# Kernel tuning notes

Hardware: AMD Instinct MI355X
Metric: run time of the kernel (lower is better)

The kernel has to match this reference:

```python
import jax, jax.numpy as jnp
import numpy as np

B, C, T, N, KS = 32, 64, 12, 1024, 3
OUT = 64


def _gconv_layer(x, Lk, theta, b):
    # x: [B, i, T, N], Lk: [ks, N, N], theta: [i, c, ks], b: [1, c, 1, 1]
    x_c = jnp.einsum('knm,bitm->bitkn', Lk, x)        # graph diffusion
    x_gc = jnp.einsum('iok,bitkn->botn', theta, x_c) + b  # channel mix + bias
    return jax.nn.relu(x_gc + x)                      # residual + relu


def setup_inputs() -> dict:
    key = jax.random.key(0)
    ks = jax.random.split(key, 8)
    return {
        'x': jax.random.normal(ks[0], (B, C, T, N), dtype=jnp.float32),
        'Lk': jax.random.normal(ks[1], (KS, N, N), dtype=jnp.float32) * 0.05,
        'theta1': jax.random.normal(ks[2], (C, C, KS), dtype=jnp.float32) * 0.1,
        'b1': jax.random.normal(ks[3], (1, C, 1, 1), dtype=jnp.float32) * 0.1,
        'theta2': jax.random.normal(ks[4], (C, C, KS), dtype=jnp.float32) * 0.1,
        'b2': jax.random.normal(ks[5], (1, C, 1, 1), dtype=jnp.float32) * 0.1,
        'fc_w': jax.random.normal(ks[6], (OUT, C), dtype=jnp.float32) * 0.1,
        'fc_b': jax.random.normal(ks[7], (OUT,), dtype=jnp.float32) * 0.1,
    }


def reference(x, Lk, theta1, b1, theta2, b2, fc_w, fc_b):
    x1 = _gconv_layer(x, Lk, theta1, b1)
    x2 = _gconv_layer(x1, Lk, theta2, b2)
    # permute [B, c, T, N] -> [B, T, N, c], then Linear(c -> OUT)
    x2 = jnp.transpose(x2, (0, 2, 3, 1))
    return x2 @ fc_w.T + fc_b
```

## Files before the change

kernel.cpp:

```cpp
#include <hip/hip_runtime.h>

typedef unsigned short ushort_t;
typedef unsigned long long u64;
typedef short short8 __attribute__((ext_vector_type(8)));
typedef float f32x4 __attribute__((ext_vector_type(4)));

#define B_   32
#define C_   64
#define T_   12
#define N_   1024
#define KS_  3
#define KC_  3072
#define RPB  768
#define NT_  48
#define BM_  192
#define LBUF 57344
#define ABYT 24576
#define BPLN 16384

__device__ __forceinline__ float bf2f(ushort_t u) {
  union { unsigned u; float f; } v; v.u = ((unsigned)u) << 16; return v.f;
}
__device__ __forceinline__ ushort_t f2bf(float f) {
  union { float f; unsigned u; } v; v.f = f;
  unsigned r = v.u + 0x7FFFu + ((v.u >> 16) & 1u);
  return (ushort_t)(r >> 16);
}

__device__ __forceinline__ void gload16(const ushort_t* g, ushort_t* l) {
  __builtin_amdgcn_global_load_lds(
      (const __attribute__((address_space(1))) unsigned int*)g,
      (__attribute__((address_space(3))) unsigned int*)l, 16, 0, 0);
}

__global__ void prep_th(const float* __restrict__ th1, const float* __restrict__ th2,
                        ushort_t* __restrict__ out) {
  int id = blockIdx.x * 256 + threadIdx.x;
  if (id >= 24576) return;
  int l = id / 12288, rem = id % 12288;
  int k = rem / 4096;
  int o = (rem >> 6) & 63;
  int i = rem & 63;
  const float* th = l ? th2 : th1;
  out[id] = f2bf(th[(i * 64 + o) * 3 + k]);
}

__global__ void prep_bt(const float* __restrict__ Lk, ushort_t* __restrict__ Bt) {
  int id = blockIdx.x * 256 + threadIdx.x;
  int k = id >> 17, rem = id & 131071;
  int n = rem >> 7, mc = rem & 127;
  int m = mc << 3;
  const float* src = Lk + ((k * N_ + n) * N_ + m);
  float4 v0 = *(const float4*)src;
  float4 v1 = *(const float4*)(src + 4);
  short8 o8;
  o8[0] = (short)f2bf(v0.x); o8[1] = (short)f2bf(v0.y);
  o8[2] = (short)f2bf(v0.z); o8[3] = (short)f2bf(v0.w);
  o8[4] = (short)f2bf(v1.x); o8[5] = (short)f2bf(v1.y);
  o8[6] = (short)f2bf(v1.z); o8[7] = (short)f2bf(v1.w);
  *(short8*)&Bt[n * KC_ + k * N_ + m] = o8;
}

template<int IN_BF16>
__global__ __launch_bounds__(256, 2)
void mix_mfma(const void* __restrict__ in, const ushort_t* __restrict__ thA,
              ushort_t* __restrict__ Y, int b0) {
  const int bid = blockIdx.x;
  const int mq = bid & 3;
  const int bt = bid >> 2;
  const int bl = bt / 12, t = bt % 12;
  const int b = b0 + bl;
  const int tid = threadIdx.x;
  const int wv = tid >> 6, lane = tid & 63;
  const int l15 = lane & 15, l4 = lane >> 4;
  const int m0 = mq * 256 + wv * 64;

  const ushort_t* xg_b = (const ushort_t*)in;
  const float*    xg_f = (const float*)in;

  short8 bfr[4][2];
  #pragma unroll
  for (int mf = 0; mf < 4; ++mf) {
    const int m = m0 + mf * 16 + l15;
    #pragma unroll
    for (int ks = 0; ks < 2; ++ks) {
      #pragma unroll
      for (int j = 0; j < 8; ++j) {
        const int i = ks * 32 + l4 * 8 + j;
        const size_t adr = ((size_t)(b * C_ + i) * T_ + t) * N_ + m;
        ushort_t v = IN_BF16 ? xg_b[adr] : f2bf(xg_f[adr]);
        bfr[mf][ks][j] = (short)v;
      }
    }
  }

  const size_t rbase = (size_t)(bt * C_);
  #pragma unroll
  for (int k = 0; k < 3; ++k) {
    short8 afr[4][2];
    #pragma unroll
    for (int of = 0; of < 4; ++of)
      #pragma unroll
      for (int ks = 0; ks < 2; ++ks)
        afr[of][ks] = *(const short8*)&thA[(size_t)(k * 64 + of * 16 + l15) * 64 + ks * 32 + l4 * 8];

    f32x4 acc[4][4] = {};
    #pragma unroll
    for (int ks = 0; ks < 2; ++ks)
      #pragma unroll
      for (int of = 0; of < 4; ++of)
        #pragma unroll
        for (int mf = 0; mf < 4; ++mf)
          acc[of][mf] = __builtin_amdgcn_mfma_f32_16x16x32_bf16(afr[of][ks], bfr[mf][ks], acc[of][mf], 0, 0, 0);

    #pragma unroll
    for (int of = 0; of < 4; ++of)
      #pragma unroll
      for (int mf = 0; mf < 4; ++mf)
        #pragma unroll
        for (int r = 0; r < 4; ++r) {
          const int o = of * 16 + l4 * 4 + r;
          Y[(rbase + o) * KC_ + k * N_ + m0 + mf * 16 + l15] = f2bf(acc[of][mf][r]);
        }
  }
}


#define MFMA12G(g, A, Bv)                                                                       \
  acc[3*(g)+0][0] = __builtin_amdgcn_mfma_f32_16x16x32_bf16(A[0], Bv[0], acc[3*(g)+0][0],0,0,0); \
  acc[3*(g)+0][1] = __builtin_amdgcn_mfma_f32_16x16x32_bf16(A[0], Bv[1], acc[3*(g)+0][1],0,0,0); \
  acc[3*(g)+0][2] = __builtin_amdgcn_mfma_f32_16x16x32_bf16(A[0], Bv[2], acc[3*(g)+0][2],0,0,0); \
  acc[3*(g)+0][3] = __builtin_amdgcn_mfma_f32_16x16x32_bf16(A[0], Bv[3], acc[3*(g)+0][3],0,0,0); \
  acc[3*(g)+1][0] = __builtin_amdgcn_mfma_f32_16x16x32_bf16(A[1], Bv[0], acc[3*(g)+1][0],0,0,0); \
  acc[3*(g)+1][1] = __builtin_amdgcn_mfma_f32_16x16x32_bf16(A[1], Bv[1], acc[3*(g)+1][1],0,0,0); \
  acc[3*(g)+1][2] = __builtin_amdgcn_mfma_f32_16x16x32_bf16(A[1], Bv[2], acc[3*(g)+1][2],0,0,0); \
  acc[3*(g)+1][3] = __builtin_amdgcn_mfma_f32_16x16x32_bf16(A[1], Bv[3], acc[3*(g)+1][3],0,0,0); \
  acc[3*(g)+2][0] = __builtin_amdgcn_mfma_f32_16x16x32_bf16(A[2], Bv[0], acc[3*(g)+2][0],0,0,0); \
  acc[3*(g)+2][1] = __builtin_amdgcn_mfma_f32_16x16x32_bf16(A[2], Bv[1], acc[3*(g)+2][1],0,0,0); \
  acc[3*(g)+2][2] = __builtin_amdgcn_mfma_f32_16x16x32_bf16(A[2], Bv[2], acc[3*(g)+2][2],0,0,0); \
  acc[3*(g)+2][3] = __builtin_amdgcn_mfma_f32_16x16x32_bf16(A[2], Bv[3], acc[3*(g)+2][3],0,0,0);

#define STAGE_A(kt, j) gload16(gA##j + (size_t)(kt) * 64,                                   \
    (ushort_t*)(lp + (((kt) & 1) ? LBUF : 0) + (j) * 8192 + wofs))
#define STAGE_B(kt, j) gload16(gB##j + (size_t)(kt) * 64,                                   \
    (ushort_t*)(lp + (((kt) & 1) ? LBUF : 0) + ABYT + (j) * 8192 + wofs))

#define LD8(p) (*(const short8*)(p))

template<int RES_BF16>
__global__ __launch_bounds__(512, 2)
void gemm8p(const ushort_t* __restrict__ Y, const ushort_t* __restrict__ Bt,
            const void* __restrict__ res, const float* __restrict__ bias,
            ushort_t* __restrict__ outb, int batch0) {
  const int nwg = gridDim.x;
  int orig = blockIdx.x;
  int q8 = nwg >> 3;
  int wg = (orig & 7) * q8 + (orig >> 3);
  const int mtile = wg >> 2, ntile = wg & 3;

  const int tid = threadIdx.x;
  const int wid = tid >> 6, lane = tid & 63;
  const int wm = wid >> 2, wn = wid & 3;
  const int l15 = lane & 15, l4 = lane >> 4;

  __shared__ ushort_t LDSU[LBUF];
  char* lp = (char*)LDSU;

  const int row0 = mtile * BM_;
  const int n0 = ntile * 256;
  const int wofs = wid * 1024;

  const int lam = lane >> 2, lc = lane & 3;
  const ushort_t *gA0, *gA1, *gA2, *gB0, *gB1, *gB2, *gB3;
  {
    int p, s, row, colel;
    p = 0 * 128 + wid * 16 + lam; s = p >= 192 ? 1 : 0; row = p - s * 192;
    colel = (lc * 8) ^ (((row >> 3) & 1) << 4);
    gA0 = Y + (size_t)(row0 + row) * KC_ + s * 32 + colel;
    p = 1 * 128 + wid * 16 + lam; s = p >= 192 ? 1 : 0; row = p - s * 192;
    colel = (lc * 8) ^ (((row >> 3) & 1) << 4);
    gA1 = Y + (size_t)(row0 + row) * KC_ + s * 32 + colel;
    p = 2 * 128 + wid * 16 + lam; s = p >= 192 ? 1 : 0; row = p - s * 192;
    colel = (lc * 8) ^ (((row >> 3) & 1) << 4);
    gA2 = Y + (size_t)(row0 + row) * KC_ + s * 32 + colel;
    p = 0 * 128 + wid * 16 + lam; s = p >> 8; row = p & 255;
    colel = (lc * 8) ^ (((row >> 3) & 1) << 4);
    gB0 = Bt + (size_t)(n0 + row) * KC_ + s * 32 + colel;
    p = 1 * 128 + wid * 16 + lam; s = p >> 8; row = p & 255;
    colel = (lc * 8) ^ (((row >> 3) & 1) << 4);
    gB1 = Bt + (size_t)(n0 + row) * KC_ + s * 32 + colel;
    p = 2 * 128 + wid * 16 + lam; s = p >> 8; row = p & 255;
    colel = (lc * 8) ^ (((row >> 3) & 1) << 4);
    gB2 = Bt + (size_t)(n0 + row) * KC_ + s * 32 + colel;
    p = 3 * 128 + wid * 16 + lam; s = p >> 8; row = p & 255;
    colel = (lc * 8) ^ (((row >> 3) & 1) << 4);
    gB3 = Bt + (size_t)(n0 + row) * KC_ + s * 32 + colel;
  }

  const int swz = ((l15 >> 3) & 1) << 5;
  const int a_base = (wm * 16 + l15) * 64 + ((l4 * 16) ^ swz);
  const int b_base = ABYT + (wn * 16 + l15) * 64 + ((l4 * 16) ^ swz);

  STAGE_B(0, 0); STAGE_B(0, 1); STAGE_B(0, 2); STAGE_B(0, 3);
  STAGE_A(0, 0); STAGE_A(0, 1); STAGE_A(0, 2);
  STAGE_B(1, 0); STAGE_B(1, 1); STAGE_B(1, 2); STAGE_B(1, 3);
  STAGE_A(1, 0); STAGE_A(1, 1);
  asm volatile("s_waitcnt vmcnt(6)" ::: "memory");
  __builtin_amdgcn_s_barrier();
  __builtin_amdgcn_sched_barrier(0);

  f32x4 acc[6][4] = {};
  short8 aA[3], aB[3], bS0[4], bS1[4];

  {
    const char* abp = lp + a_base;
    const char* bbp = lp + b_base;
    aA[0] = LD8(abp);          aA[1] = LD8(abp + 2048);   aA[2] = LD8(abp + 4096);
    bS0[0] = LD8(bbp);         bS0[1] = LD8(bbp + 4096);
    bS0[2] = LD8(bbp + 8192);  bS0[3] = LD8(bbp + 12288);
  }

  for (int u = 0; u < NT_; ++u) {
    const char* abp = lp + ((u & 1) ? LBUF : 0) + a_base;
    const char* bbp = lp + ((u & 1) ? LBUF : 0) + b_base;
    const char* abn = lp + ((u & 1) ? 0 : LBUF) + a_base;
    const char* bbn = lp + ((u & 1) ? 0 : LBUF) + b_base;

    {
      if (u + 1 < NT_) STAGE_A(u + 1, 2);
      __builtin_amdgcn_s_barrier();
      __builtin_amdgcn_sched_barrier(0);
      aB[0] = LD8(abp + 6144); aB[1] = LD8(abp + 8192); aB[2] = LD8(abp + 10240);
      __builtin_amdgcn_sched_barrier(0);
      __builtin_amdgcn_s_setprio(1);
      MFMA12G(0, aA, bS0)
      __builtin_amdgcn_s_setprio(0);
      __builtin_amdgcn_s_barrier();
    }
    {
      if (u + 2 < NT_) { STAGE_B(u + 2, 0); STAGE_B(u + 2, 1); }
      __builtin_amdgcn_s_barrier();
      __builtin_amdgcn_sched_barrier(0);
      aA[0] = LD8(abp + 12288);         aA[1] = LD8(abp + 12288 + 2048);
      aA[2] = LD8(abp + 12288 + 4096);
      bS1[0] = LD8(bbp + BPLN);         bS1[1] = LD8(bbp + BPLN + 4096);
      bS1[2] = LD8(bbp + BPLN + 8192);  bS1[3] = LD8(bbp + BPLN + 12288);
      __builtin_amdgcn_sched_barrier(0);
      __builtin_amdgcn_s_setprio(1);
      MFMA12G(1, aB, bS0)
      __builtin_amdgcn_s_setprio(0);
      __builtin_amdgcn_s_barrier();
    }
    {
      __builtin_amdgcn_s_barrier();
      __builtin_amdgcn_sched_barrier(0);
      aB[0] = LD8(abp + 12288 + 6144);
      aB[1] = LD8(abp + 12288 + 8192);
      aB[2] = LD8(abp + 12288 + 10240);
      __builtin_amdgcn_sched_barrier(0);
      __builtin_amdgcn_s_setprio(1);
      MFMA12G(0, aA, bS1)
      __builtin_amdgcn_s_setprio(0);
      __builtin_amdgcn_s_barrier();
    }
    {
      if (u + 2 < NT_) {
        STAGE_B(u + 2, 2); STAGE_B(u + 2, 3);
        STAGE_A(u + 2, 0); STAGE_A(u + 2, 1);
        asm volatile("s_waitcnt vmcnt(6)" ::: "memory");
      } else if (u + 2 == NT_) {
        asm volatile("s_waitcnt vmcnt(0)" ::: "memory");
      }
      __builtin_amdgcn_s_barrier();
      __builtin_amdgcn_sched_barrier(0);
      if (u + 1 < NT_) {
        aA[0] = LD8(abn);          aA[1] = LD8(abn + 2048);   aA[2] = LD8(abn + 4096);
        bS0[0] = LD8(bbn);         bS0[1] = LD8(bbn + 4096);
        bS0[2] = LD8(bbn + 8192);  bS0[3] = LD8(bbn + 12288);
      }
      __builtin_amdgcn_sched_barrier(0);
      __builtin_amdgcn_s_setprio(1);
      MFMA12G(1, aB, bS1)
      __builtin_amdgcn_s_setprio(0);
      __builtin_amdgcn_s_barrier();
    }
  }

  const float*    resf = (const float*)res;
  const ushort_t* resb = (const ushort_t*)res;
  const int gb = batch0 + (mtile >> 2);
  const int rowb0 = (mtile & 3) * BM_;
  const int colb = n0 + wn * 16 + l15;
  #pragma unroll
  for (int mf = 0; mf < 6; ++mf) {
    #pragma unroll
    for (int r = 0; r < 4; ++r) {
      int rl = mf * 32 + wm * 16 + l4 * 4 + r;
      int rowb = rowb0 + rl;
      int t = rowb >> 6, o = rowb & 63;
      float bs = bias[o];
      size_t base = ((size_t)(gb * C_ + o) * T_ + t) * N_;
      #pragma unroll
      for (int nf = 0; nf < 4; ++nf) {
        int col = colb + nf * 64;
        float rv = RES_BF16 ? bf2f(resb[base + col]) : resf[base + col];
        float v = acc[mf][nf][r] + bs + rv;
        v = fmaxf(v, 0.0f);
        outb[base + col] = f2bf(v);
      }
    }
  }
}

__global__ __launch_bounds__(256, 2)
void fc_mfma(const ushort_t* __restrict__ x2, const float* __restrict__ fw,
             const float* __restrict__ fb, float* __restrict__ out) {
  const int tid = threadIdx.x;
  const int wv = tid >> 6, lane = tid & 63;
  const int l15 = lane & 15, l4 = lane >> 4;
  const int row0 = blockIdx.x * 256 + wv * 64;

  short8 wfr[4][2];
  #pragma unroll
  for (int nf = 0; nf < 4; ++nf) {
    const float* wsrc = fw + (nf * 16 + l15) * 64;
    #pragma unroll
    for (int ks = 0; ks < 2; ++ks) {
      float4 wa = *(const float4*)(wsrc + ks * 32 + l4 * 8);
      float4 wb = *(const float4*)(wsrc + ks * 32 + l4 * 8 + 4);
      short8 w8;
      w8[0] = (short)f2bf(wa.x); w8[1] = (short)f2bf(wa.y);
      w8[2] = (short)f2bf(wa.z); w8[3] = (short)f2bf(wa.w);
      w8[4] = (short)f2bf(wb.x); w8[5] = (short)f2bf(wb.y);
      w8[6] = (short)f2bf(wb.z); w8[7] = (short)f2bf(wb.w);
      wfr[nf][ks] = w8;
    }
  }

  f32x4 acc[4][4] = {};
  #pragma unroll
  for (int mf = 0; mf < 4; ++mf) {
    const int row = row0 + mf * 16 + l15;
    const int n = row & 1023, tb = row >> 10;
    const int b = tb / 12, t = tb - b * 12;
    const size_t base = ((size_t)(b * 768) + t) * 1024 + n;
    #pragma unroll
    for (int ks = 0; ks < 2; ++ks) {
      short8 af;
      #pragma unroll
      for (int j = 0; j < 8; ++j) {
        const int o = ks * 32 + l4 * 8 + j;
        af[j] = (short)x2[base + (size_t)o * 12288];
      }
      #pragma unroll
      for (int nf = 0; nf < 4; ++nf)
        acc[mf][nf] = __builtin_amdgcn_mfma_f32_16x16x32_bf16(af, wfr[nf][ks], acc[mf][nf], 0, 0, 0);
    }
  }

  #pragma unroll
  for (int mf = 0; mf < 4; ++mf)
    #pragma unroll
    for (int nf = 0; nf < 4; ++nf) {
      const float fbv = fb[nf * 16 + l15];
      #pragma unroll
      for (int r = 0; r < 4; ++r)
        out[(size_t)(row0 + mf * 16 + l4 * 4 + r) * 64 + nf * 16 + l15] = acc[mf][nf][r] + fbv;
    }
}

extern "C" void kernel_launch(void* const* d_in, const int* in_sizes, int n_in,
                              void* d_out, int out_size, void* d_ws, size_t ws_size,
                              hipStream_t stream) {
  const float* x   = (const float*)d_in[0];
  const float* Lk  = (const float*)d_in[1];
  const float* th1 = (const float*)d_in[2];
  const float* b1  = (const float*)d_in[3];
  const float* th2 = (const float*)d_in[4];
  const float* b2  = (const float*)d_in[5];
  const float* fcw = (const float*)d_in[6];
  const float* fcb = (const float*)d_in[7];

  char* ws = (char*)d_ws;
  size_t off = 0;
  auto alloc = [&](size_t bytes) { size_t p = off; off += (bytes + 255) & ~(size_t)255; return p; };
  size_t oBt = alloc((size_t)KC_ * N_ * 2);
  size_t oTh = alloc((size_t)2 * 3 * 64 * 64 * 2);
  size_t oX2 = alloc((size_t)B_ * C_ * T_ * N_ * 2);
  size_t perB = (size_t)RPB * KC_ * 2;
  size_t avail = ws_size > off ? ws_size - off : 0;
  int NB = (int)(avail / perB);
  if (NB > B_) NB = B_;
  if (NB < 1) NB = 1;

  ushort_t* Bt = (ushort_t*)(ws + oBt);
  ushort_t* Th = (ushort_t*)(ws + oTh);
  ushort_t* X2 = (ushort_t*)(ws + oX2);
  ushort_t* Yb = (ushort_t*)(ws + off);
  ushort_t* X1 = (ushort_t*)d_out;

  prep_th<<<96, 256, 0, stream>>>(th1, th2, Th);
  prep_bt<<<1536, 256, 0, stream>>>(Lk, Bt);

  for (int b0 = 0; b0 < B_; b0 += NB) {
    int nb = (b0 + NB <= B_) ? NB : (B_ - b0);
    mix_mfma<0><<<nb * 48, 256, 0, stream>>>((const void*)x, Th, Yb, b0);
    gemm8p<0><<<dim3(16 * nb), 512, 0, stream>>>(Yb, Bt, (const void*)x, b1, X1, b0);
  }
  for (int b0 = 0; b0 < B_; b0 += NB) {
    int nb = (b0 + NB <= B_) ? NB : (B_ - b0);
    mix_mfma<1><<<nb * 48, 256, 0, stream>>>((const void*)X1, Th + 12288, Yb, b0);
    gemm8p<1><<<dim3(16 * nb), 512, 0, stream>>>(Yb, Bt, (const void*)X1, b2, X2, b0);
  }
  fc_mfma<<<1536, 256, 0, stream>>>(X2, fcw, fcb, (float*)d_out);
}
```

Before: 480.8 us.

## Fuse next-layer channel mix and final FC into graph-conv GEMM epilogues

Layer-1's GEMM epilogue now writes the relu'd tile into LDS and immediately runs layer 2's theta channel-mix MFMA on it, producing the second Y buffer directly. Layer 2's epilogue likewise applies the FC linear in-kernel and writes the final float output. This removes the separate mix_mfma pass for layer 2, the X2 round trip and the fc_mfma kernel, interleaving both layers per batch chunk. In exchange it drops the occupancy hint in launch bounds, raises register and LDS pressure in the epilogue, and needs two Y buffers so fewer batches fit per chunk.

```diff
diff --git a/kernel.cpp b/kernel.cpp
--- a/kernel.cpp
+++ b/kernel.cpp
@@ -61,9 +61,8 @@
   *(short8*)&Bt[n * KC_ + k * N_ + m] = o8;
 }
 
-template<int IN_BF16>
 __global__ __launch_bounds__(256, 2)
-void mix_mfma(const void* __restrict__ in, const ushort_t* __restrict__ thA,
+void mix_mfma(const float* __restrict__ xg_f, const ushort_t* __restrict__ thA,
               ushort_t* __restrict__ Y, int b0) {
   const int bid = blockIdx.x;
   const int mq = bid & 3;
@@ -75,9 +74,6 @@
   const int l15 = lane & 15, l4 = lane >> 4;
   const int m0 = mq * 256 + wv * 64;
 
-  const ushort_t* xg_b = (const ushort_t*)in;
-  const float*    xg_f = (const float*)in;
-
   short8 bfr[4][2];
   #pragma unroll
   for (int mf = 0; mf < 4; ++mf) {
@@ -88,8 +84,7 @@
       for (int j = 0; j < 8; ++j) {
         const int i = ks * 32 + l4 * 8 + j;
         const size_t adr = ((size_t)(b * C_ + i) * T_ + t) * N_ + m;
-        ushort_t v = IN_BF16 ? xg_b[adr] : f2bf(xg_f[adr]);
-        bfr[mf][ks][j] = (short)v;
+        bfr[mf][ks][j] = (short)f2bf(xg_f[adr]);
       }
     }
   }
@@ -147,11 +142,15 @@
 
 #define LD8(p) (*(const short8*)(p))
 
-template<int RES_BF16>
-__global__ __launch_bounds__(512, 2)
+template<int LAYER>
+__global__ __launch_bounds__(512)
 void gemm8p(const ushort_t* __restrict__ Y, const ushort_t* __restrict__ Bt,
             const void* __restrict__ res, const float* __restrict__ bias,
-            ushort_t* __restrict__ outb, int batch0) {
+            ushort_t* __restrict__ x1out,
+            const void* __restrict__ wgt,
+            const float* __restrict__ fb,
+            void* __restrict__ fout,
+            int batch0) {
   const int nwg = gridDim.x;
   int orig = blockIdx.x;
   int q8 = nwg >> 3;
@@ -290,83 +289,129 @@
   const ushort_t* resb = (const ushort_t*)res;
   const int gb = batch0 + (mtile >> 2);
   const int rowb0 = (mtile & 3) * BM_;
-  const int colb = n0 + wn * 16 + l15;
+  const int tloc = (mtile & 3) * 3;
   #pragma unroll
   for (int mf = 0; mf < 6; ++mf) {
-    #pragma unroll
-    for (int r = 0; r < 4; ++r) {
-      int rl = mf * 32 + wm * 16 + l4 * 4 + r;
-      int rowb = rowb0 + rl;
-      int t = rowb >> 6, o = rowb & 63;
-      float bs = bias[o];
-      size_t base = ((size_t)(gb * C_ + o) * T_ + t) * N_;
-      #pragma unroll
-      for (int nf = 0; nf < 4; ++nf) {
-        int col = colb + nf * 64;
-        float rv = RES_BF16 ? bf2f(resb[base + col]) : resf[base + col];
-        float v = acc[mf][nf][r] + bs + rv;
-        v = fmaxf(v, 0.0f);
-        outb[base + col] = f2bf(v);
+    const int rl0 = mf * 32 + wm * 16 + l4 * 4;
+    const int btl = rl0 >> 6;
+    const int i0  = rl0 & 63;
+    #pragma unroll
+    for (int nf = 0; nf < 4; ++nf) {
+      const int nl = wn * 16 + nf * 64 + l15;
+      const int col = n0 + nl;
+      u64 pack = 0;
+      #pragma unroll
+      for (int r = 0; r < 4; ++r) {
+        int rowb = rowb0 + rl0 + r;
+        int t = rowb >> 6, o = rowb & 63;
+        size_t base = ((size_t)(gb * C_ + o) * T_ + t) * N_;
+        float rv = (LAYER == 0) ? resf[base + col] : bf2f(resb[base + col]);
+        float v = fmaxf(acc[mf][nf][r] + bias[o] + rv, 0.0f);
+        ushort_t bv = f2bf(v);
+        if (LAYER == 0) x1out[base + col] = bv;
+        pack |= (u64)bv << (16 * r);
       }
-    }
-  }
-}
-
-__global__ __launch_bounds__(256, 2)
-void fc_mfma(const ushort_t* __restrict__ x2, const float* __restrict__ fw,
-             const float* __restrict__ fb, float* __restrict__ out) {
-  const int tid = threadIdx.x;
-  const int wv = tid >> 6, lane = tid & 63;
-  const int l15 = lane & 15, l4 = lane >> 4;
-  const int row0 = blockIdx.x * 256 + wv * 64;
-
-  short8 wfr[4][2];
-  #pragma unroll
-  for (int nf = 0; nf < 4; ++nf) {
-    const float* wsrc = fw + (nf * 16 + l15) * 64;
-    #pragma unroll
-    for (int ks = 0; ks < 2; ++ks) {
-      float4 wa = *(const float4*)(wsrc + ks * 32 + l4 * 8);
-      float4 wb = *(const float4*)(wsrc + ks * 32 + l4 * 8 + 4);
-      short8 w8;
-      w8[0] = (short)f2bf(wa.x); w8[1] = (short)f2bf(wa.y);
-      w8[2] = (short)f2bf(wa.z); w8[3] = (short)f2bf(wa.w);
-      w8[4] = (short)f2bf(wb.x); w8[5] = (short)f2bf(wb.y);
-      w8[6] = (short)f2bf(wb.z); w8[7] = (short)f2bf(wb.w);
-      wfr[nf][ks] = w8;
-    }
-  }
-
-  f32x4 acc[4][4] = {};
-  #pragma unroll
-  for (int mf = 0; mf < 4; ++mf) {
-    const int row = row0 + mf * 16 + l15;
-    const int n = row & 1023, tb = row >> 10;
-    const int b = tb / 12, t = tb - b * 12;
-    const size_t base = ((size_t)(b * 768) + t) * 1024 + n;
-    #pragma unroll
-    for (int ks = 0; ks < 2; ++ks) {
-      short8 af;
-      #pragma unroll
-      for (int j = 0; j < 8; ++j) {
-        const int o = ks * 32 + l4 * 8 + j;
-        af[j] = (short)x2[base + (size_t)o * 12288];
+      int byte = btl * 32768 + nl * 128 + i0 * 2;
+      byte ^= ((nl & 7) << 4);
+      *(u64*)(lp + byte) = pack;
+    }
+  }
+  asm volatile("s_waitcnt lgkmcnt(0)" ::: "memory");
+  __builtin_amdgcn_sched_barrier(0);
+  __builtin_amdgcn_s_barrier();
+
+  if (LAYER == 0) {
+    const ushort_t* th2 = (const ushort_t*)wgt;
+    ushort_t* y2 = (ushort_t*)fout;
+    const int y2tb = (mtile >> 2) * RPB + tloc * 64;
+    #pragma unroll
+    for (int kk = 0; kk < 3; ++kk) {
+      short8 afr[2][2];
+      #pragma unroll
+      for (int f = 0; f < 2; ++f)
+        #pragma unroll
+        for (int ks = 0; ks < 2; ++ks)
+          afr[f][ks] = *(const short8*)&th2[((size_t)kk * 64 + (wm * 2 + f) * 16 + l15) * 64 + ks * 32 + l4 * 8];
+      f32x4 a2[3][2][4] = {};
+      #pragma unroll
+      for (int bt = 0; bt < 3; ++bt)
+        #pragma unroll
+        for (int ks = 0; ks < 2; ++ks)
+          #pragma unroll
+          for (int nf = 0; nf < 4; ++nf) {
+            const int nl = wn * 16 + nf * 64 + l15;
+            int byte = bt * 32768 + nl * 128 + (ks * 32 + l4 * 8) * 2;
+            byte ^= ((nl & 7) << 4);
+            short8 bfr = LD8(lp + byte);
+            #pragma unroll
+            for (int f = 0; f < 2; ++f)
+              a2[bt][f][nf] = __builtin_amdgcn_mfma_f32_16x16x32_bf16(afr[f][ks], bfr, a2[bt][f][nf], 0, 0, 0);
+          }
+      #pragma unroll
+      for (int bt = 0; bt < 3; ++bt)
+        #pragma unroll
+        for (int f = 0; f < 2; ++f)
+          #pragma unroll
+          for (int nf = 0; nf < 4; ++nf) {
+            const int m = n0 + wn * 16 + nf * 64 + l15;
+            const int o2b = (wm * 2 + f) * 16 + l4 * 4;
+            const size_t rbase = (size_t)(y2tb + bt * 64 + o2b);
+            #pragma unroll
+            for (int r = 0; r < 4; ++r)
+              y2[(rbase + r) * KC_ + kk * N_ + m] = f2bf(a2[bt][f][nf][r]);
+          }
+    }
+  } else {
+    const float* fw = (const float*)wgt;
+    float* outf = (float*)fout;
+    short8 afr[2][2];
+    #pragma unroll
+    for (int f = 0; f < 2; ++f)
+      #pragma unroll
+      for (int ks = 0; ks < 2; ++ks) {
+        const float* wsrc = fw + ((wm * 2 + f) * 16 + l15) * 64 + ks * 32 + l4 * 8;
+        float4 wa = *(const float4*)wsrc;
+        float4 wb = *(const float4*)(wsrc + 4);
+        short8 w8;
+        w8[0] = (short)f2bf(wa.x); w8[1] = (short)f2bf(wa.y);
+        w8[2] = (short)f2bf(wa.z); w8[3] = (short)f2bf(wa.w);
+        w8[4] = (short)f2bf(wb.x); w8[5] = (short)f2bf(wb.y);
+        w8[6] = (short)f2bf(wb.z); w8[7] = (short)f2bf(wb.w);
+        afr[f][ks] = w8;
       }
-      #pragma unroll
-      for (int nf = 0; nf < 4; ++nf)
-        acc[mf][nf] = __builtin_amdgcn_mfma_f32_16x16x32_bf16(af, wfr[nf][ks], acc[mf][nf], 0, 0, 0);
-    }
-  }
-
-  #pragma unroll
-  for (int mf = 0; mf < 4; ++mf)
-    #pragma unroll
-    for (int nf = 0; nf < 4; ++nf) {
-      const float fbv = fb[nf * 16 + l15];
-      #pragma unroll
-      for (int r = 0; r < 4; ++r)
-        out[(size_t)(row0 + mf * 16 + l4 * 4 + r) * 64 + nf * 16 + l15] = acc[mf][nf][r] + fbv;
-    }
+    f32x4 a2[3][2][4] = {};
+    #pragma unroll
+    for (int bt = 0; bt < 3; ++bt)
+      #pragma unroll
+      for (int ks = 0; ks < 2; ++ks)
+        #pragma unroll
+        for (int nf = 0; nf < 4; ++nf) {
+          const int nl = wn * 16 + nf * 64 + l15;
+          int byte = bt * 32768 + nl * 128 + (ks * 32 + l4 * 8) * 2;
+          byte ^= ((nl & 7) << 4);
+          short8 bfr = LD8(lp + byte);
+          #pragma unroll
+          for (int f = 0; f < 2; ++f)
+            a2[bt][f][nf] = __builtin_amdgcn_mfma_f32_16x16x32_bf16(afr[f][ks], bfr, a2[bt][f][nf], 0, 0, 0);
+        }
+    #pragma unroll
+    for (int bt = 0; bt < 3; ++bt)
+      #pragma unroll
+      for (int f = 0; f < 2; ++f)
+        #pragma unroll
+        for (int nf = 0; nf < 4; ++nf) {
+          const int n = n0 + wn * 16 + nf * 64 + l15;
+          const int o2b = (wm * 2 + f) * 16 + l4 * 4;
+          float4 fb4 = *(const float4*)&fb[o2b];
+          const size_t btg = (size_t)(gb * 12 + tloc + bt);
+          float4 v;
+          v.x = a2[bt][f][nf][0] + fb4.x;
+          v.y = a2[bt][f][nf][1] + fb4.y;
+          v.z = a2[bt][f][nf][2] + fb4.z;
+          v.w = a2[bt][f][nf][3] + fb4.w;
+          *(float4*)&outf[(btg * 1024 + n) * 64 + o2b] = v;
+        }
+  }
 }
 
 extern "C" void kernel_launch(void* const* d_in, const int* in_sizes, int n_in,
@@ -386,31 +431,28 @@
   auto alloc = [&](size_t bytes) { size_t p = off; off += (bytes + 255) & ~(size_t)255; return p; };
   size_t oBt = alloc((size_t)KC_ * N_ * 2);
   size_t oTh = alloc((size_t)2 * 3 * 64 * 64 * 2);
-  size_t oX2 = alloc((size_t)B_ * C_ * T_ * N_ * 2);
-  size_t perB = (size_t)RPB * KC_ * 2;
+  size_t oX1 = alloc((size_t)B_ * C_ * T_ * N_ * 2);
+  size_t perY = (size_t)RPB * KC_ * 2;
   size_t avail = ws_size > off ? ws_size - off : 0;
-  int NB = (int)(avail / perB);
+  int NB = (int)(avail / (2 * perY));
   if (NB > B_) NB = B_;
   if (NB < 1) NB = 1;
 
-  ushort_t* Bt = (ushort_t*)(ws + oBt);
-  ushort_t* Th = (ushort_t*)(ws + oTh);
-  ushort_t* X2 = (ushort_t*)(ws + oX2);
-  ushort_t* Yb = (ushort_t*)(ws + off);
-  ushort_t* X1 = (ushort_t*)d_out;
+  ushort_t* Bt  = (ushort_t*)(ws + oBt);
+  ushort_t* Th  = (ushort_t*)(ws + oTh);
+  ushort_t* X1  = (ushort_t*)(ws + oX1);
+  ushort_t* Yb1 = (ushort_t*)(ws + off);
+  ushort_t* Yb2 = Yb1 + (size_t)NB * RPB * KC_;
 
   prep_th<<<96, 256, 0, stream>>>(th1, th2, Th);
   prep_bt<<<1536, 256, 0, stream>>>(Lk, Bt);
 
   for (int b0 = 0; b0 < B_; b0 += NB) {
     int nb = (b0 + NB <= B_) ? NB : (B_ - b0);
-    mix_mfma<0><<<nb * 48, 256, 0, stream>>>((const void*)x, Th, Yb, b0);
-    gemm8p<0><<<dim3(16 * nb), 512, 0, stream>>>(Yb, Bt, (const void*)x, b1, X1, b0);
-  }
-  for (int b0 = 0; b0 < B_; b0 += NB) {
-    int nb = (b0 + NB <= B_) ? NB : (B_ - b0);
-    mix_mfma<1><<<nb * 48, 256, 0, stream>>>((const void*)X1, Th + 12288, Yb, b0);
-    gemm8p<1><<<dim3(16 * nb), 512, 0, stream>>>(Yb, Bt, (const void*)X1, b2, X2, b0);
-  }
-  fc_mfma<<<1536, 256, 0, stream>>>(X2, fcw, fcb, (float*)d_out);
-}
+    mix_mfma<<<nb * 48, 256, 0, stream>>>(x, Th, Yb1, b0);
+    gemm8p<0><<<dim3(16 * nb), 512, 0, stream>>>(
+        Yb1, Bt, (const void*)x, b1, X1, (const void*)(Th + 12288), fcb, (void*)Yb2, b0);
+    gemm8p<1><<<dim3(16 * nb), 512, 0, stream>>>(
+        Yb2, Bt, (const void*)X1, b2, X1, (const void*)fcw, fcb, d_out, b0);
+  }
+}
```

Result: faster. 444.4 us (-7.6%).
